# Kernel tuning notes

Measured on AMD Instinct MI355X. Metric: run time of the kernel, lower is better.

Reference implementation:

```python
import jax, jax.numpy as jnp
import numpy as np

N = 100000   # num nodes
E = 1000000  # num edges
IN, H, OUT = 128, 64, 64
THR = 0.1      # lcs_threshold
LN_EPS = 1e-5


def setup_inputs() -> dict:
    key = jax.random.key(0)
    ks = jax.random.split(key, 8)
    x = jax.random.normal(ks[0], (N, IN), dtype=jnp.float32)
    edge_index = jax.random.randint(ks[1], (2, E), 0, N, dtype=jnp.int32)
    W1 = jax.random.normal(ks[2], (IN, H), dtype=jnp.float32) / np.float32(np.sqrt(IN))
    b1 = jnp.zeros((H,), jnp.float32)
    W2 = jax.random.normal(ks[3], (H, OUT), dtype=jnp.float32) / np.float32(np.sqrt(H))
    b2 = jnp.zeros((OUT,), jnp.float32)
    ln_gamma = jnp.ones((H,), jnp.float32)
    ln_beta = jnp.zeros((H,), jnp.float32)
    return {"x": x, "W1": W1, "b1": b1, "W2": W2, "b2": b2,
            "ln_gamma": ln_gamma, "ln_beta": ln_beta, "edge_index": edge_index}


def _gcn_conv(h_in, W, b, src, dst, ew, n):
    """PyG GCNConv: D^-1/2 (A+I) D^-1/2 (h_in @ W) + b, with edge weights ew.
    Masked edges (ew=0) contribute neither messages nor degree -> equivalent to
    filtering them out."""
    h = h_in @ W                                   # [n, d_out]
    deg = jax.ops.segment_sum(ew, dst, num_segments=n) + 1.0  # +1 self-loop
    dis = jax.lax.rsqrt(deg)                       # deg >= 1, finite
    norm = dis[src] * dis[dst] * ew                # [E]
    agg = jax.ops.segment_sum(h[src] * norm[:, None], dst, num_segments=n)
    agg = agg + h * (dis * dis)[:, None]           # self-loop term
    return agg + b


def _layer_norm(h, gamma, beta):
    mu = jnp.mean(h, axis=-1, keepdims=True)
    var = jnp.mean(jnp.square(h - mu), axis=-1, keepdims=True)
    return (h - mu) * jax.lax.rsqrt(var + LN_EPS) * gamma + beta


def reference(x, W1, b1, W2, b2, ln_gamma, ln_beta, edge_index):
    src, dst = edge_index[0], edge_index[1]
    n = x.shape[0]
    ones_e = jnp.ones((src.shape[0],), x.dtype)

    # layer 0: no LCS filtering (i == 0)
    h = _gcn_conv(x, W1, b1, src, dst, ones_e, n)
    h = _layer_norm(h, ln_gamma, ln_beta)
    h = jax.nn.relu(h)  # dropout: inference mode (identity)

    # layer 1: LCS filtering via node scores = min-max normalized L2 norm
    s = jnp.linalg.norm(h, axis=1)
    s = (s - s.min()) / (s.max() - s.min() + 1e-8)
    mask = (s[dst] > THR).astype(x.dtype)

    out = _gcn_conv(h, W2, b2, src, dst, mask, n)
    return jax.nn.log_softmax(out, axis=1)
```

## Files before the change

kernel.cpp:

```cpp
#include <hip/hip_runtime.h>
#include <math.h>

#define N_NODES 100000
#define N_EDGES 1000000
#define IN_F 128
#define H_F 64
#define THRV 0.1f
#define LN_EPS 1e-5f
#define GRID_AGG 2048

#define BSHIFT 9
#define NB 196
#define EPB 2048
#define NPB ((N_EDGES + EPB - 1) / EPB)

static __device__ __forceinline__ float wave_sum(float x) {
  for (int o = 32; o > 0; o >>= 1) x += __shfl_xor(x, o, 64);
  return x;
}
static __device__ __forceinline__ float wave_max(float x) {
  for (int o = 32; o > 0; o >>= 1) x = fmaxf(x, __shfl_xor(x, o, 64));
  return x;
}


__global__ __launch_bounds__(256) void k_bcount(const int* __restrict__ dst,
                                                int* __restrict__ bcnt) {
  __shared__ int h[NB];
  for (int i = threadIdx.x; i < NB; i += 256) h[i] = 0;
  __syncthreads();
  int base = blockIdx.x * EPB;
  for (int i = threadIdx.x; i < EPB; i += 256) {
    int e = base + i;
    if (e < N_EDGES) atomicAdd(&h[dst[e] >> BSHIFT], 1);
  }
  __syncthreads();
  for (int i = threadIdx.x; i < NB; i += 256)
    if (h[i]) atomicAdd(&bcnt[i], h[i]);
}

__global__ void k_bscan(const int* __restrict__ bcnt, int* __restrict__ bbase,
                        int* __restrict__ bcur) {
  __shared__ int lds[256];
  int t = threadIdx.x;
  int v = (t < NB) ? bcnt[t] : 0;
  lds[t] = v;
  __syncthreads();
  int val = v;
  for (int o = 1; o < 256; o <<= 1) {
    int y = (t >= o) ? lds[t - o] : 0;
    __syncthreads();
    val += y;
    lds[t] = val;
    __syncthreads();
  }
  if (t < NB) {
    int ex = val - v;
    bbase[t] = ex;
    bcur[t] = ex;
  }
  if (t == 255) bbase[NB] = val;
}

__global__ __launch_bounds__(256) void k_part(const int* __restrict__ src,
                                              const int* __restrict__ dst,
                                              int* __restrict__ bcur,
                                              int* __restrict__ part) {
  __shared__ int h[NB];
  __shared__ int cur[NB];
  for (int i = threadIdx.x; i < NB; i += 256) h[i] = 0;
  __syncthreads();
  int base = blockIdx.x * EPB;
  for (int i = threadIdx.x; i < EPB; i += 256) {
    int e = base + i;
    if (e < N_EDGES) atomicAdd(&h[dst[e] >> BSHIFT], 1);
  }
  __syncthreads();
  for (int i = threadIdx.x; i < NB; i += 256) {
    int c = h[i];
    cur[i] = c ? atomicAdd(&bcur[i], c) : 0;
  }
  __syncthreads();
  for (int i = threadIdx.x; i < EPB; i += 256) {
    int e = base + i;
    if (e < N_EDGES) {
      int d = dst[e];
      int b = d >> BSHIFT;
      int pos = atomicAdd(&cur[b], 1);
      part[pos] = src[e] | ((d & 511) << 17);
    }
  }
}

__global__ __launch_bounds__(256) void k_build(
    const int* __restrict__ part, const int* __restrict__ bbase,
    int* __restrict__ indeg, int* __restrict__ offs, float* __restrict__ dis1,
    int* __restrict__ csr_src) {
  __shared__ int cnt[512];
  __shared__ int slds[256];
  int b = blockIdx.x;
  int t = threadIdx.x;
  int beg = bbase[b], end = bbase[b + 1];
  for (int i = t; i < 512; i += 256) cnt[i] = 0;
  __syncthreads();
  for (int i = beg + t; i < end; i += 256)
    atomicAdd(&cnt[(part[i] >> 17) & 511], 1);
  __syncthreads();
  int a0 = cnt[2 * t], a1 = cnt[2 * t + 1];
  int pairsum = a0 + a1;
  slds[t] = pairsum;
  __syncthreads();
  int val = pairsum;
  for (int o = 1; o < 256; o <<= 1) {
    int y = (t >= o) ? slds[t - o] : 0;
    __syncthreads();
    val += y;
    slds[t] = val;
    __syncthreads();
  }
  int ex = val - pairsum;
  int off0 = ex, off1 = ex + a0;
  cnt[2 * t] = off0;
  cnt[2 * t + 1] = off1;
  int node0 = (b << BSHIFT) + 2 * t;
  if (node0 < N_NODES) {
    indeg[node0] = a0;
    offs[node0] = beg + off0;
    dis1[node0] = rsqrtf((float)a0 + 1.f);
  }
  if (node0 + 1 < N_NODES) {
    indeg[node0 + 1] = a1;
    offs[node0 + 1] = beg + off1;
    dis1[node0 + 1] = rsqrtf((float)a1 + 1.f);
  }
  __syncthreads();
  for (int i = beg + t; i < end; i += 256) {
    int p = part[i];
    int loc = (p >> 17) & 511;
    int pos = atomicAdd(&cnt[loc], 1);
    csr_src[beg + pos] = p & 131071;
  }
}

template <int K>
__global__ __launch_bounds__(256) void k_gemm(const float* __restrict__ X,
                                              const float* __restrict__ W,
                                              const float* __restrict__ scale,
                                              float* __restrict__ Y, int nrows) {
  constexpr int C4 = K / 4;
  __shared__ __align__(16) float Xs[64][K];
  __shared__ __align__(16) float Ws[K][64];
  int t = threadIdx.x;
  int rbase = blockIdx.x * 64;
  for (int idx = t; idx < 64 * C4; idx += 256) {
    int row = idx / C4;
    int c4 = idx % C4;
    int gr = rbase + row;
    if (gr >= nrows) gr = nrows - 1;
    float4 v = *(const float4*)(X + (size_t)gr * K + c4 * 4);
    int c4s = c4 ^ (row & 7);
    *(float4*)&Xs[row][c4s * 4] = v;
  }
  for (int idx = t; idx < K * 16; idx += 256) {
    ((float4*)&Ws[0][0])[idx] = ((const float4*)W)[idx];
  }
  __syncthreads();

  int tx = t & 15, ty = t >> 4;
  int r0 = ty * 4, c0 = tx * 4;
  float acc[4][4] = {};
#pragma unroll 8
  for (int k = 0; k < K; k += 4) {
    float xv[4][4], wv[4][4];
#pragma unroll
    for (int i = 0; i < 4; ++i) {
      int r = r0 + i;
      int c4s = ((k >> 2) ^ (r & 7)) << 2;
      *(float4*)xv[i] = *(const float4*)&Xs[r][c4s];
    }
#pragma unroll
    for (int j = 0; j < 4; ++j)
      *(float4*)wv[j] = *(const float4*)&Ws[k + j][c0];
#pragma unroll
    for (int i = 0; i < 4; ++i)
#pragma unroll
      for (int kk = 0; kk < 4; ++kk)
#pragma unroll
        for (int j = 0; j < 4; ++j)
          acc[i][j] = fmaf(xv[i][kk], wv[kk][j], acc[i][j]);
  }
#pragma unroll
  for (int i = 0; i < 4; ++i) {
    int gr = rbase + r0 + i;
    if (gr < nrows) {
      float sc = scale[gr];
      float4 o;
      o.x = acc[i][0] * sc;
      o.y = acc[i][1] * sc;
      o.z = acc[i][2] * sc;
      o.w = acc[i][3] * sc;
      *(float4*)(Y + (size_t)gr * 64 + c0) = o;
    }
  }
}

__global__ __launch_bounds__(256) void k_agg1(
    const float* __restrict__ h1p, const int* __restrict__ offs,
    const int* __restrict__ indeg, const int* __restrict__ csr_src,
    const float* __restrict__ dis1, const float* __restrict__ b1,
    const float* __restrict__ gamma, const float* __restrict__ beta,
    float* __restrict__ h, float* __restrict__ s, float* __restrict__ mmpart) {
  int lane = threadIdx.x & 63;
  int wid = blockIdx.x * 4 + (threadIdx.x >> 6);
  int nw = gridDim.x * 4;
  float bmin = __builtin_inff(), bmax = -__builtin_inff();
  for (int v = wid; v < N_NODES; v += nw) {
    int beg = offs[v];
    int deg = indeg[v];
    float disv = dis1[v];
    float acc = h1p[v * 64 + lane];
    for (int c = 0; c < deg; c += 64) {
      int m = deg - c;
      if (m > 64) m = 64;
      int ul = (lane < m) ? csr_src[beg + c + lane] : 0;
      int j = 0;
      for (; j + 8 <= m; j += 8) {
        int u0 = __shfl(ul, j + 0), u1 = __shfl(ul, j + 1);
        int u2 = __shfl(ul, j + 2), u3 = __shfl(ul, j + 3);
        int u4 = __shfl(ul, j + 4), u5 = __shfl(ul, j + 5);
        int u6 = __shfl(ul, j + 6), u7 = __shfl(ul, j + 7);
        float a0 = h1p[u0 * 64 + lane], a1 = h1p[u1 * 64 + lane];
        float a2 = h1p[u2 * 64 + lane], a3 = h1p[u3 * 64 + lane];
        float a4 = h1p[u4 * 64 + lane], a5 = h1p[u5 * 64 + lane];
        float a6 = h1p[u6 * 64 + lane], a7 = h1p[u7 * 64 + lane];
        acc += ((a0 + a1) + (a2 + a3)) + ((a4 + a5) + (a6 + a7));
      }
      for (; j < m; ++j) {
        int u = __shfl(ul, j);
        acc += h1p[u * 64 + lane];
      }
    }
    acc = disv * acc + b1[lane];
    float mu = wave_sum(acc) * (1.f / 64.f);
    float d = acc - mu;
    float var = wave_sum(d * d) * (1.f / 64.f);
    float hn = d * rsqrtf(var + LN_EPS) * gamma[lane] + beta[lane];
    hn = fmaxf(hn, 0.f);
    h[v * 64 + lane] = hn;
    float sv = sqrtf(wave_sum(hn * hn));
    if (lane == 0) s[v] = sv;
    bmin = fminf(bmin, sv);
    bmax = fmaxf(bmax, sv);
  }
  __shared__ float lmin[4], lmax[4];
  if ((threadIdx.x & 63) == 0) {
    lmin[threadIdx.x >> 6] = bmin;
    lmax[threadIdx.x >> 6] = bmax;
  }
  __syncthreads();
  if (threadIdx.x == 0) {
    mmpart[blockIdx.x * 2] = fminf(fminf(lmin[0], lmin[1]), fminf(lmin[2], lmin[3]));
    mmpart[blockIdx.x * 2 + 1] = fmaxf(fmaxf(lmax[0], lmax[1]), fmaxf(lmax[2], lmax[3]));
  }
}

__global__ void k_minmax2(const float* __restrict__ mmpart, float* __restrict__ smm,
                          int nblk) {
  int t = threadIdx.x;
  float mn = __builtin_inff(), mx = -__builtin_inff();
  for (int i = t; i < nblk; i += 256) {
    mn = fminf(mn, mmpart[i * 2]);
    mx = fmaxf(mx, mmpart[i * 2 + 1]);
  }
  for (int o = 32; o; o >>= 1) {
    mn = fminf(mn, __shfl_xor(mn, o, 64));
    mx = fmaxf(mx, __shfl_xor(mx, o, 64));
  }
  __shared__ float a[4], b[4];
  if ((t & 63) == 0) { a[t >> 6] = mn; b[t >> 6] = mx; }
  __syncthreads();
  if (t == 0) {
    smm[0] = fminf(fminf(a[0], a[1]), fminf(a[2], a[3]));
    smm[1] = fmaxf(fmaxf(b[0], b[1]), fmaxf(b[2], b[3]));
  }
}

__global__ void k_dis2(const float* __restrict__ s, const float* __restrict__ smm,
                       const int* __restrict__ indeg, float* __restrict__ dis2) {
  int v = blockIdx.x * blockDim.x + threadIdx.x;
  if (v < N_NODES) {
    float inv = 1.f / (smm[1] - smm[0] + 1e-8f);
    float sn = (s[v] - smm[0]) * inv;
    float d = (sn > THRV) ? (float)indeg[v] : 0.f;
    dis2[v] = rsqrtf(d + 1.f);
  }
}

__global__ __launch_bounds__(256) void k_agg2(
    const float* __restrict__ h2p, const int* __restrict__ offs,
    const int* __restrict__ indeg, const int* __restrict__ csr_src,
    const float* __restrict__ s, const float* __restrict__ smm,
    const float* __restrict__ dis2, const float* __restrict__ b2,
    float* __restrict__ out) {
  int lane = threadIdx.x & 63;
  int wid = blockIdx.x * 4 + (threadIdx.x >> 6);
  int nw = gridDim.x * 4;
  float smin = smm[0];
  float inv = 1.f / (smm[1] - smm[0] + 1e-8f);
  for (int v = wid; v < N_NODES; v += nw) {
    float disv = dis2[v];
    float sn = (s[v] - smin) * inv;
    float acc = h2p[v * 64 + lane];
    if (sn > THRV) {
      int beg = offs[v];
      int deg = indeg[v];
      for (int c = 0; c < deg; c += 64) {
        int m = deg - c;
        if (m > 64) m = 64;
        int ul = (lane < m) ? csr_src[beg + c + lane] : 0;
        int j = 0;
        for (; j + 8 <= m; j += 8) {
          int u0 = __shfl(ul, j + 0), u1 = __shfl(ul, j + 1);
          int u2 = __shfl(ul, j + 2), u3 = __shfl(ul, j + 3);
          int u4 = __shfl(ul, j + 4), u5 = __shfl(ul, j + 5);
          int u6 = __shfl(ul, j + 6), u7 = __shfl(ul, j + 7);
          float a0 = h2p[u0 * 64 + lane], a1 = h2p[u1 * 64 + lane];
          float a2 = h2p[u2 * 64 + lane], a3 = h2p[u3 * 64 + lane];
          float a4 = h2p[u4 * 64 + lane], a5 = h2p[u5 * 64 + lane];
          float a6 = h2p[u6 * 64 + lane], a7 = h2p[u7 * 64 + lane];
          acc += ((a0 + a1) + (a2 + a3)) + ((a4 + a5) + (a6 + a7));
        }
        for (; j < m; ++j) {
          int u = __shfl(ul, j);
          acc += h2p[u * 64 + lane];
        }
      }
    }
    acc = disv * acc + b2[lane];
    float m = wave_max(acc);
    float p = expf(acc - m);
    float sum = wave_sum(p);
    out[v * 64 + lane] = acc - m - logf(sum);
  }
}

extern "C" void kernel_launch(void* const* d_in, const int* in_sizes, int n_in,
                              void* d_out, int out_size, void* d_ws, size_t ws_size,
                              hipStream_t stream) {
  const float* x = (const float*)d_in[0];
  const float* W1 = (const float*)d_in[1];
  const float* b1 = (const float*)d_in[2];
  const float* W2 = (const float*)d_in[3];
  const float* b2 = (const float*)d_in[4];
  const float* gamma = (const float*)d_in[5];
  const float* beta = (const float*)d_in[6];
  const int* ei = (const int*)d_in[7];
  const int* src = ei;
  const int* dst = ei + N_EDGES;
  float* out = (float*)d_out;

  char* ws = (char*)d_ws;
  size_t off = 0;
  auto alloc = [&](size_t bytes) {
    void* p = ws + off;
    off += (bytes + 255) & ~(size_t)255;
    return p;
  };
  int* indeg = (int*)alloc(N_NODES * 4);
  int* offs = (int*)alloc(N_NODES * 4);
  int* bcnt = (int*)alloc(NB * 4);
  int* bbase = (int*)alloc((NB + 1) * 4);
  int* bcur = (int*)alloc(NB * 4);
  int* csr_src = (int*)alloc(N_EDGES * 4);
  float* s = (float*)alloc(N_NODES * 4);
  float* dis1 = (float*)alloc(N_NODES * 4);
  float* dis2 = (float*)alloc(N_NODES * 4);
  float* mmpart = (float*)alloc(GRID_AGG * 2 * 4);
  float* smm = (float*)alloc(256);
  float* h1 = (float*)alloc((size_t)N_NODES * 64 * 4);
  float* h = (float*)alloc((size_t)N_NODES * 64 * 4);
  int* part = (int*)h1;
  (void)ws_size;
  (void)n_in;
  (void)in_sizes;
  (void)out_size;

  hipMemsetAsync(bcnt, 0, NB * 4, stream);
  k_bcount<<<NPB, 256, 0, stream>>>(dst, bcnt);
  k_bscan<<<1, 256, 0, stream>>>(bcnt, bbase, bcur);
  k_part<<<NPB, 256, 0, stream>>>(src, dst, bcur, part);
  k_build<<<NB, 256, 0, stream>>>(part, bbase, indeg, offs, dis1, csr_src);
  int gemm_grid = (N_NODES + 63) / 64;
  k_gemm<IN_F><<<gemm_grid, 256, 0, stream>>>(x, W1, dis1, h1, N_NODES);
  k_agg1<<<GRID_AGG, 256, 0, stream>>>(h1, offs, indeg, csr_src, dis1, b1, gamma,
                                       beta, h, s, mmpart);
  k_minmax2<<<1, 256, 0, stream>>>(mmpart, smm, GRID_AGG);
  k_dis2<<<(N_NODES + 255) / 256, 256, 0, stream>>>(s, smm, indeg, dis2);
  k_gemm<H_F><<<gemm_grid, 256, 0, stream>>>(h, W2, dis2, h1 , N_NODES);
  k_agg2<<<GRID_AGG, 256, 0, stream>>>(h1, offs, indeg, csr_src, s, smm, dis2, b2,
                                       out);
}
```

Measured before the change: 244.1 us.

## Double-buffer GEMM K-chunks with async global-to-LDS loads

Restructures the dense GEMM kernel to load X and W in 32-wide K chunks into double-buffered shared memory using direct global-to-LDS async loads, so the next chunk is prefetched while the current one is computed. This is meant to overlap memory latency with FMAs and to cut LDS footprint, which may raise occupancy. It adds per-chunk barriers and waitcnt syncs, and it relies on the lane-to-address mapping of the LDS-direct load builtin being right.

```diff
diff --git a/kernel.cpp b/kernel.cpp
--- a/kernel.cpp
+++ b/kernel.cpp
@@ -21,6 +21,12 @@
 static __device__ __forceinline__ float wave_max(float x) {
   for (int o = 32; o > 0; o >>= 1) x = fmaxf(x, __shfl_xor(x, o, 64));
   return x;
+}
+
+static __device__ __forceinline__ void async16(const void* g, void* l) {
+  __builtin_amdgcn_global_load_lds(
+      (const __attribute__((address_space(1))) void*)g,
+      (__attribute__((address_space(3))) void*)l, 16, 0, 0);
 }
 
 
@@ -147,48 +153,71 @@
                                               const float* __restrict__ W,
                                               const float* __restrict__ scale,
                                               float* __restrict__ Y, int nrows) {
-  constexpr int C4 = K / 4;
-  __shared__ __align__(16) float Xs[64][K];
-  __shared__ __align__(16) float Ws[K][64];
+  constexpr int KC = 32;
+  constexpr int NCH = K / KC;
+  __shared__ __align__(16) float Xs[2][64][KC];
+  __shared__ __align__(16) float Ws[2][KC][64];
   int t = threadIdx.x;
   int rbase = blockIdx.x * 64;
-  for (int idx = t; idx < 64 * C4; idx += 256) {
-    int row = idx / C4;
-    int c4 = idx % C4;
-    int gr = rbase + row;
-    if (gr >= nrows) gr = nrows - 1;
-    float4 v = *(const float4*)(X + (size_t)gr * K + c4 * 4);
-    int c4s = c4 ^ (row & 7);
-    *(float4*)&Xs[row][c4s * 4] = v;
-  }
-  for (int idx = t; idx < K * 16; idx += 256) {
-    ((float4*)&Ws[0][0])[idx] = ((const float4*)W)[idx];
-  }
+  int wid = t >> 6, l = t & 63;
+  int p0 = wid * 2, p1 = p0 + 1;
+
+  int xrow0 = p0 * 8 + (l >> 3);
+  int xrow1 = p1 * 8 + (l >> 3);
+  int gr0 = rbase + xrow0;
+  int gr1 = rbase + xrow1;
+  if (gr0 >= nrows) gr0 = nrows - 1;
+  if (gr1 >= nrows) gr1 = nrows - 1;
+  const float* xg0 = X + (size_t)gr0 * K + (((l & 7) ^ (xrow0 & 7)) << 2);
+  const float* xg1 = X + (size_t)gr1 * K + (((l & 7) ^ (xrow1 & 7)) << 2);
+  const float* wg0 = W + (size_t)(p0 * 4 + (l >> 4)) * 64 + ((l & 15) << 2);
+  const float* wg1 = W + (size_t)(p1 * 4 + (l >> 4)) * 64 + ((l & 15) << 2);
+
+#define STAGE(b, c)                                                   \
+  do {                                                                \
+    async16(xg0 + (c)*KC, (char*)&Xs[b][0][0] + p0 * 1024);           \
+    async16(xg1 + (c)*KC, (char*)&Xs[b][0][0] + p1 * 1024);           \
+    async16(wg0 + (size_t)(c)*KC * 64, (char*)&Ws[b][0][0] + p0 * 1024); \
+    async16(wg1 + (size_t)(c)*KC * 64, (char*)&Ws[b][0][0] + p1 * 1024); \
+  } while (0)
+
+  STAGE(0, 0);
+  asm volatile("s_waitcnt vmcnt(0)" ::: "memory");
   __syncthreads();
 
   int tx = t & 15, ty = t >> 4;
   int r0 = ty * 4, c0 = tx * 4;
   float acc[4][4] = {};
-#pragma unroll 8
-  for (int k = 0; k < K; k += 4) {
-    float xv[4][4], wv[4][4];
-#pragma unroll
-    for (int i = 0; i < 4; ++i) {
-      int r = r0 + i;
-      int c4s = ((k >> 2) ^ (r & 7)) << 2;
-      *(float4*)xv[i] = *(const float4*)&Xs[r][c4s];
-    }
-#pragma unroll
-    for (int j = 0; j < 4; ++j)
-      *(float4*)wv[j] = *(const float4*)&Ws[k + j][c0];
-#pragma unroll
-    for (int i = 0; i < 4; ++i)
-#pragma unroll
-      for (int kk = 0; kk < 4; ++kk)
-#pragma unroll
-        for (int j = 0; j < 4; ++j)
-          acc[i][j] = fmaf(xv[i][kk], wv[kk][j], acc[i][j]);
-  }
+
+  for (int c = 0; c < NCH; ++c) {
+    int cur = c & 1;
+    if (c + 1 < NCH) STAGE(cur ^ 1, c + 1);
+#pragma unroll
+    for (int k = 0; k < KC; k += 4) {
+      float xv[4][4], wv[4][4];
+#pragma unroll
+      for (int i = 0; i < 4; ++i) {
+        int r = r0 + i;
+        *(float4*)xv[i] = *(const float4*)&Xs[cur][r][(((k >> 2) ^ (r & 7))) << 2];
+      }
+#pragma unroll
+      for (int j = 0; j < 4; ++j)
+        *(float4*)wv[j] = *(const float4*)&Ws[cur][k + j][c0];
+#pragma unroll
+      for (int i = 0; i < 4; ++i)
+#pragma unroll
+        for (int kk = 0; kk < 4; ++kk)
+#pragma unroll
+          for (int j = 0; j < 4; ++j)
+            acc[i][j] = fmaf(xv[i][kk], wv[kk][j], acc[i][j]);
+    }
+    if (c + 1 < NCH) {
+      asm volatile("s_waitcnt vmcnt(0)" ::: "memory");
+      __syncthreads();
+    }
+  }
+#undef STAGE
+
 #pragma unroll
   for (int i = 0; i < 4; ++i) {
     int gr = rbase + r0 + i;
```

After: 239.0 us. -2.1%, faster.
